# Performance work log

Measured on AMD Instinct MI355X. Metric: run time of the kernel, lower is better.

## Reference

```python
import jax, jax.numpy as jnp
import numpy as np

BLOCK_SIZE = 5
DROP_RATE = 0.5


def setup_inputs() -> dict:
    key = jax.random.key(0)
    k1, k2 = jax.random.split(key)
    B, C, H, W = 64, 128, 56, 56
    bs = BLOCK_SIZE
    x = jax.random.normal(k1, (B, C, H, W), dtype=jnp.float32)
    # uniform noise used to realize the Bernoulli(gamma) sample deterministically
    u = jax.random.uniform(k2, (B, C, H - bs + 1, W - bs + 1), dtype=jnp.float32)
    return {"x": x, "u": u, "num_batches_tracked": 1}


def reference(x, u, num_batches_tracked):
    bs = BLOCK_SIZE
    B, C, H, W = x.shape
    # keep-rate schedule (num_batches_tracked is a Python int => static)
    keep_rate = max(1.0 - DROP_RATE / 20000.0 * num_batches_tracked, 1.0 - DROP_RATE)
    gamma = (1.0 - keep_rate) / bs ** 2 * W ** 2 / (W - bs + 1) ** 2
    # Bernoulli(gamma) sample on the valid (H-bs+1, W-bs+1) grid
    mask = (u < gamma).astype(x.dtype)
    # The original scatters 1s at offsets 0..bs-1 around each sampled point into
    # a padded (H, W) mask. That is exactly a bs x bs max-pool dilation with
    # (bs-1, bs-1) zero padding on each spatial side, producing an (H, W) output.
    dilated = jax.lax.reduce_window(
        mask, 0.0, jax.lax.max,
        window_dimensions=(1, 1, bs, bs),
        window_strides=(1, 1, 1, 1),
        padding=((0, 0), (0, 0), (bs - 1, bs - 1), (bs - 1, bs - 1)),
    )
    block_mask = 1.0 - dilated  # (B, C, H, W)
    countM = block_mask.size
    count_ones = block_mask.sum()
    dind = (countM / count_ones) * block_mask
    return x * dind
```

## Files before the change

kernel.cpp:

```cpp
#include <hip/hip_runtime.h>

namespace {
constexpr int BSZ = 5;
constexpr int Bn = 64, Cn = 128, Hn = 56, Wn = 56;
constexpr long long NX = (long long)Bn * Cn * Hn * Wn;
constexpr long long NU = (long long)Bn * Cn * 52 * 52;
constexpr int PLANE_U = 52 * 52;
constexpr int PLANE_X4 = 784;
constexpr int MAXH = 8192;
constexpr int NU4 = (int)(NU / 4);
constexpr int NX4 = (int)(NX / 4);
constexpr int SCAN_BLOCKS = NU4 / 1024;
constexpr int MUL_BLOCKS  = NX4 / 1024;

struct Ctl {
  unsigned int nhits;
  unsigned int pad0;
  float scale;
  unsigned int hits[MAXH];
};

__device__ __forceinline__ void record_hits(float4 v, int idx4, float g, Ctl* ctl) {
  if (v.x < g || v.y < g || v.z < g || v.w < g) {
    unsigned int b = (unsigned int)(4 * idx4);
    if (v.x < g) { unsigned int p = atomicAdd(&ctl->nhits, 1u); if (p < MAXH) ctl->hits[p] = b + 0u; }
    if (v.y < g) { unsigned int p = atomicAdd(&ctl->nhits, 1u); if (p < MAXH) ctl->hits[p] = b + 1u; }
    if (v.z < g) { unsigned int p = atomicAdd(&ctl->nhits, 1u); if (p < MAXH) ctl->hits[p] = b + 2u; }
    if (v.w < g) { unsigned int p = atomicAdd(&ctl->nhits, 1u); if (p < MAXH) ctl->hits[p] = b + 3u; }
  }
}

__device__ __forceinline__ void apply_hit(float4& a, int p, int row, int c0,
                                          int hp, int hi, int hj) {
  if (hp == p && row >= hi && row <= hi + 4) {
    if (c0 + 0 >= hj && c0 + 0 <= hj + 4) a.x = 0.0f;
    if (c0 + 1 >= hj && c0 + 1 <= hj + 4) a.y = 0.0f;
    if (c0 + 2 >= hj && c0 + 2 <= hj + 4) a.z = 0.0f;
    if (c0 + 3 >= hj && c0 + 3 <= hj + 4) a.w = 0.0f;
  }
}
}

__global__ __launch_bounds__(256) void k_scan(const float4* __restrict__ u4,
                                              const int* __restrict__ nbt,
                                              Ctl* __restrict__ ctl) {
  double kr = 1.0 - 0.5 / 20000.0 * (double)nbt[0];
  if (kr < 0.5) kr = 0.5;
  double gd = (1.0 - kr) / (double)(BSZ * BSZ) * (double)(Wn * Wn) /
              (double)((Wn - BSZ + 1) * (Wn - BSZ + 1));
  const float g = (float)gd;

  const int base = blockIdx.x * 1024 + threadIdx.x;
  float4 v0 = u4[base];
  float4 v1 = u4[base + 256];
  float4 v2 = u4[base + 512];
  float4 v3 = u4[base + 768];
  record_hits(v0, base, g, ctl);
  record_hits(v1, base + 256, g, ctl);
  record_hits(v2, base + 512, g, ctl);
  record_hits(v3, base + 768, g, ctl);
}

__global__ void k_count(Ctl* ctl) {
  __shared__ unsigned int s_total;
  if (threadIdx.x == 0) s_total = 0u;
  __syncthreads();
  const int n = (int)min(ctl->nhits, (unsigned int)MAXH);
  unsigned int local = 0;
  for (int t = threadIdx.x; t < n * 25; t += blockDim.x) {
    const int hi = t / 25;
    const int cell = t - hi * 25;
    const unsigned int e = ctl->hits[hi];
    const int plane = (int)(e / PLANE_U);
    const int rem = (int)(e - (unsigned int)plane * PLANE_U);
    const int i = rem / 52;
    const int j = rem - i * 52;
    const int hh = i + cell / 5;
    const int ww = j + cell % 5;
    bool covered = false;
    for (int p = 0; p < hi; ++p) {
      const unsigned int e2 = ctl->hits[p];
      const int pl2 = (int)(e2 / PLANE_U);
      if (pl2 != plane) continue;
      const int rem2 = (int)(e2 - (unsigned int)pl2 * PLANE_U);
      const int i2 = rem2 / 52;
      const int j2 = rem2 - i2 * 52;
      if (hh >= i2 && hh <= i2 + 4 && ww >= j2 && ww <= j2 + 4) { covered = true; break; }
    }
    if (!covered) local++;
  }
  if (local) atomicAdd(&s_total, local);
  __syncthreads();
  if (threadIdx.x == 0) {
    double count_ones = (double)NX - (double)s_total;
    ctl->scale = (float)((double)NX / count_ones);
  }
}

__global__ __launch_bounds__(256) void k_mul(const float4* __restrict__ x4,
                                             float4* __restrict__ o4,
                                             const Ctl* __restrict__ ctl) {
  const int blockStart = blockIdx.x * 1024;
  const int base = blockStart + threadIdx.x;
  float4 a0 = x4[base];
  float4 a1 = x4[base + 256];
  float4 a2 = x4[base + 512];
  float4 a3 = x4[base + 768];

  const float s = ctl->scale;
  a0.x *= s; a0.y *= s; a0.z *= s; a0.w *= s;
  a1.x *= s; a1.y *= s; a1.z *= s; a1.w *= s;
  a2.x *= s; a2.y *= s; a2.z *= s; a2.w *= s;
  a3.x *= s; a3.y *= s; a3.z *= s; a3.w *= s;

  const int n = (int)min(ctl->nhits, (unsigned int)MAXH);
  const int pmin = blockStart / PLANE_X4;
  const int pmax = (blockStart + 1023) / PLANE_X4;
  bool any = false;
  for (int h0 = 0; h0 < n; h0 += 64) {
    const int h = h0 + (int)(threadIdx.x & 63);
    bool mine = false;
    if (h < n) {
      const int hp = (int)(ctl->hits[h] / (unsigned int)PLANE_U);
      mine = (hp >= pmin && hp <= pmax);
    }
    if (__any(mine)) { any = true; break; }
  }
  if (any) {
    const int f1 = base + 256, f2 = base + 512, f3 = base + 768;
    const int p0 = base / PLANE_X4, p1 = f1 / PLANE_X4, p2 = f2 / PLANE_X4, p3 = f3 / PLANE_X4;
    const int r0 = base - p0 * PLANE_X4, r1 = f1 - p1 * PLANE_X4,
              r2 = f2 - p2 * PLANE_X4, r3 = f3 - p3 * PLANE_X4;
    const int row0 = r0 / 14, row1 = r1 / 14, row2 = r2 / 14, row3 = r3 / 14;
    const int c00 = (r0 - row0 * 14) * 4, c01 = (r1 - row1 * 14) * 4,
              c02 = (r2 - row2 * 14) * 4, c03 = (r3 - row3 * 14) * 4;
    for (int h = 0; h < n; ++h) {
      const unsigned int e = ctl->hits[h];
      const int hp = (int)(e / (unsigned int)PLANE_U);
      const int rem = (int)(e - (unsigned int)hp * PLANE_U);
      const int hi = rem / 52;
      const int hj = rem - hi * 52;
      apply_hit(a0, p0, row0, c00, hp, hi, hj);
      apply_hit(a1, p1, row1, c01, hp, hi, hj);
      apply_hit(a2, p2, row2, c02, hp, hi, hj);
      apply_hit(a3, p3, row3, c03, hp, hi, hj);
    }
  }
  o4[base] = a0;
  o4[base + 256] = a1;
  o4[base + 512] = a2;
  o4[base + 768] = a3;
}

extern "C" void kernel_launch(void* const* d_in, const int* in_sizes, int n_in,
                              void* d_out, int out_size, void* d_ws, size_t ws_size,
                              hipStream_t stream) {
  const float* x = (const float*)d_in[0];
  const float* u = (const float*)d_in[1];
  const int* nbt = (const int*)d_in[2];
  float* out = (float*)d_out;
  Ctl* ctl = (Ctl*)d_ws;

  hipMemsetAsync(&ctl->nhits, 0, sizeof(unsigned int), stream);
  k_scan<<<SCAN_BLOCKS, 256, 0, stream>>>((const float4*)u, nbt, ctl);
  k_count<<<1, 256, 0, stream>>>(ctl);
  k_mul<<<MUL_BLOCKS, 256, 0, stream>>>((const float4*)x, (float4*)out, ctl);
}
```

Before: 70.11 us.

## Fuse block-count into multiply kernel and use nontemporal loads/stores

Removes the single-block k_count kernel and has every k_mul block recompute the uncovered-cell count and scale redundantly in shared memory, eliminating one launch and a serial dependency. All global loads and stores switch to nontemporal builtins on ext_vector float4. The redundant count work is O(n^2·25) per block, which with a few thousand hits could add substantial compute to each of the many blocks.

```diff
diff --git a/kernel.cpp b/kernel.cpp
--- a/kernel.cpp
+++ b/kernel.cpp
@@ -1,4 +1,6 @@
 #include <hip/hip_runtime.h>
+
+typedef float f32x4 __attribute__((ext_vector_type(4)));
 
 namespace {
 constexpr int BSZ = 5;
@@ -16,11 +18,10 @@
 struct Ctl {
   unsigned int nhits;
   unsigned int pad0;
-  float scale;
   unsigned int hits[MAXH];
 };
 
-__device__ __forceinline__ void record_hits(float4 v, int idx4, float g, Ctl* ctl) {
+__device__ __forceinline__ void record_hits(f32x4 v, int idx4, float g, Ctl* ctl) {
   if (v.x < g || v.y < g || v.z < g || v.w < g) {
     unsigned int b = (unsigned int)(4 * idx4);
     if (v.x < g) { unsigned int p = atomicAdd(&ctl->nhits, 1u); if (p < MAXH) ctl->hits[p] = b + 0u; }
@@ -30,7 +31,7 @@
   }
 }
 
-__device__ __forceinline__ void apply_hit(float4& a, int p, int row, int c0,
+__device__ __forceinline__ void apply_hit(f32x4& a, int p, int row, int c0,
                                           int hp, int hi, int hj) {
   if (hp == p && row >= hi && row <= hi + 4) {
     if (c0 + 0 >= hj && c0 + 0 <= hj + 4) a.x = 0.0f;
@@ -41,7 +42,7 @@
 }
 }
 
-__global__ __launch_bounds__(256) void k_scan(const float4* __restrict__ u4,
+__global__ __launch_bounds__(256) void k_scan(const f32x4* __restrict__ u4,
                                               const int* __restrict__ nbt,
                                               Ctl* __restrict__ ctl) {
   double kr = 1.0 - 0.5 / 20000.0 * (double)nbt[0];
@@ -51,27 +52,38 @@
   const float g = (float)gd;
 
   const int base = blockIdx.x * 1024 + threadIdx.x;
-  float4 v0 = u4[base];
-  float4 v1 = u4[base + 256];
-  float4 v2 = u4[base + 512];
-  float4 v3 = u4[base + 768];
+  f32x4 v0 = __builtin_nontemporal_load(u4 + base);
+  f32x4 v1 = __builtin_nontemporal_load(u4 + base + 256);
+  f32x4 v2 = __builtin_nontemporal_load(u4 + base + 512);
+  f32x4 v3 = __builtin_nontemporal_load(u4 + base + 768);
   record_hits(v0, base, g, ctl);
   record_hits(v1, base + 256, g, ctl);
   record_hits(v2, base + 512, g, ctl);
   record_hits(v3, base + 768, g, ctl);
 }
 
-__global__ void k_count(Ctl* ctl) {
-  __shared__ unsigned int s_total;
-  if (threadIdx.x == 0) s_total = 0u;
+__global__ __launch_bounds__(256) void k_mul(const f32x4* __restrict__ x4,
+                                             f32x4* __restrict__ o4,
+                                             const Ctl* __restrict__ ctl) {
+  const int blockStart = blockIdx.x * 1024;
+  const int base = blockStart + threadIdx.x;
+  f32x4 a0 = __builtin_nontemporal_load(x4 + base);
+  f32x4 a1 = __builtin_nontemporal_load(x4 + base + 256);
+  f32x4 a2 = __builtin_nontemporal_load(x4 + base + 512);
+  f32x4 a3 = __builtin_nontemporal_load(x4 + base + 768);
+
+  __shared__ unsigned int s_cnt;
+  __shared__ float s_scale;
+  if (threadIdx.x == 0) s_cnt = 0u;
   __syncthreads();
+
   const int n = (int)min(ctl->nhits, (unsigned int)MAXH);
   unsigned int local = 0;
-  for (int t = threadIdx.x; t < n * 25; t += blockDim.x) {
+  for (int t = (int)threadIdx.x; t < n * 25; t += 256) {
     const int hi = t / 25;
     const int cell = t - hi * 25;
     const unsigned int e = ctl->hits[hi];
-    const int plane = (int)(e / PLANE_U);
+    const int plane = (int)(e / (unsigned int)PLANE_U);
     const int rem = (int)(e - (unsigned int)plane * PLANE_U);
     const int i = rem / 52;
     const int j = rem - i * 52;
@@ -80,7 +92,7 @@
     bool covered = false;
     for (int p = 0; p < hi; ++p) {
       const unsigned int e2 = ctl->hits[p];
-      const int pl2 = (int)(e2 / PLANE_U);
+      const int pl2 = (int)(e2 / (unsigned int)PLANE_U);
       if (pl2 != plane) continue;
       const int rem2 = (int)(e2 - (unsigned int)pl2 * PLANE_U);
       const int i2 = rem2 / 52;
@@ -89,31 +101,17 @@
     }
     if (!covered) local++;
   }
-  if (local) atomicAdd(&s_total, local);
+  if (local) atomicAdd(&s_cnt, local);
   __syncthreads();
   if (threadIdx.x == 0) {
-    double count_ones = (double)NX - (double)s_total;
-    ctl->scale = (float)((double)NX / count_ones);
+    double count_ones = (double)NX - (double)s_cnt;
+    s_scale = (float)((double)NX / count_ones);
   }
-}
+  __syncthreads();
 
-__global__ __launch_bounds__(256) void k_mul(const float4* __restrict__ x4,
-                                             float4* __restrict__ o4,
-                                             const Ctl* __restrict__ ctl) {
-  const int blockStart = blockIdx.x * 1024;
-  const int base = blockStart + threadIdx.x;
-  float4 a0 = x4[base];
-  float4 a1 = x4[base + 256];
-  float4 a2 = x4[base + 512];
-  float4 a3 = x4[base + 768];
+  const float s = s_scale;
+  a0 *= s; a1 *= s; a2 *= s; a3 *= s;
 
-  const float s = ctl->scale;
-  a0.x *= s; a0.y *= s; a0.z *= s; a0.w *= s;
-  a1.x *= s; a1.y *= s; a1.z *= s; a1.w *= s;
-  a2.x *= s; a2.y *= s; a2.z *= s; a2.w *= s;
-  a3.x *= s; a3.y *= s; a3.z *= s; a3.w *= s;
-
-  const int n = (int)min(ctl->nhits, (unsigned int)MAXH);
   const int pmin = blockStart / PLANE_X4;
   const int pmax = (blockStart + 1023) / PLANE_X4;
   bool any = false;
@@ -146,10 +144,11 @@
       apply_hit(a3, p3, row3, c03, hp, hi, hj);
     }
   }
-  o4[base] = a0;
-  o4[base + 256] = a1;
-  o4[base + 512] = a2;
-  o4[base + 768] = a3;
+
+  __builtin_nontemporal_store(a0, o4 + base);
+  __builtin_nontemporal_store(a1, o4 + base + 256);
+  __builtin_nontemporal_store(a2, o4 + base + 512);
+  __builtin_nontemporal_store(a3, o4 + base + 768);
 }
 
 extern "C" void kernel_launch(void* const* d_in, const int* in_sizes, int n_in,
@@ -162,7 +161,6 @@
   Ctl* ctl = (Ctl*)d_ws;
 
   hipMemsetAsync(&ctl->nhits, 0, sizeof(unsigned int), stream);
-  k_scan<<<SCAN_BLOCKS, 256, 0, stream>>>((const float4*)u, nbt, ctl);
-  k_count<<<1, 256, 0, stream>>>(ctl);
-  k_mul<<<MUL_BLOCKS, 256, 0, stream>>>((const float4*)x, (float4*)out, ctl);
+  k_scan<<<SCAN_BLOCKS, 256, 0, stream>>>((const f32x4*)u, nbt, ctl);
+  k_mul<<<MUL_BLOCKS, 256, 0, stream>>>((const f32x4*)x, (f32x4*)out, ctl);
 }
```

After: 85.94 us. 1.23x slower.
